# Performance work log

Measured on AMD Instinct MI355X. Metric: run time of the kernel, lower is better.

The kernel has to match this reference:

```python
import jax, jax.numpy as jnp
import numpy as np

B, T, D, H = 4, 2048, 512, 8
K = D // H  # head dim = 64

def setup_inputs() -> dict:
    key = jax.random.key(0)
    k1, k2, k3, k4 = jax.random.split(key, 4)
    x = jax.random.normal(k1, (B, T, D), dtype=jnp.float32)
    # torch nn.Linear stores weight as [out_features, in_features]
    w_qkv = jax.random.normal(k2, (3 * D, D), dtype=jnp.float32) * (D ** -0.5)
    w_proj = jax.random.normal(k3, (D, D), dtype=jnp.float32) * (D ** -0.5)
    b_proj = jax.random.normal(k4, (D,), dtype=jnp.float32) * 0.01
    return {"x": x, "w_qkv": w_qkv, "w_proj": w_proj, "b_proj": b_proj}

def reference(x, w_qkv, w_proj, b_proj):
    Bx, Tx, Dx = x.shape
    # qkv projection (no bias): [B,T,3D]
    qkv = jnp.einsum('btd,ed->bte', x, w_qkv)
    q, k, v = jnp.split(qkv, 3, axis=-1)
    # [B,H,T,K]
    def heads(t):
        return t.reshape(Bx, Tx, H, K).transpose(0, 2, 1, 3)
    q, k, v = heads(q), heads(k), heads(v)
    # scaled scores with causal mask
    scores = jnp.einsum('bhqk,bhsk->bhqs', q, k) * (K ** -0.5)  # [B,H,T,T]
    causal = jnp.tril(jnp.ones((Tx, Tx), dtype=bool))
    scores = jnp.where(causal, scores, -jnp.inf)
    attn = jax.nn.softmax(scores, axis=-1)  # dropout p=0.0 -> identity
    out = jnp.einsum('bhqs,bhsk->bhqk', attn, v)  # [B,H,T,K]
    out = out.transpose(0, 2, 1, 3).reshape(Bx, Tx, Dx)
    out = jnp.einsum('btd,ed->bte', out, w_proj) + b_proj
    return out
```

## Files before the change

### kernel.cpp

```cpp
#include <hip/hip_runtime.h>


typedef unsigned short u16;
typedef __attribute__((ext_vector_type(8))) __bf16 bf16x8;
typedef __attribute__((ext_vector_type(8))) unsigned short u16x8;
typedef __attribute__((ext_vector_type(4))) float f32x4;

#define DEV static __device__ __forceinline__

DEV void async16(const u16* g, u16* l) {
  __builtin_amdgcn_global_load_lds(
      (const __attribute__((address_space(1))) unsigned int*)g,
      (__attribute__((address_space(3))) unsigned int*)l, 16, 0, 0);
}
DEV u16x8 gld8(const u16* p) { return *(const u16x8*)p; }
DEV void lst8(u16* p, u16x8 v) { *(u16x8*)p = v; }
DEV bf16x8 ldsld8(const u16* p) {
  return __builtin_bit_cast(bf16x8, *(const u16x8*)p);
}
DEV f32x4 mfma16(bf16x8 a, bf16x8 b, f32x4 c) {
  return __builtin_amdgcn_mfma_f32_16x16x32_bf16(a, b, c, 0, 0, 0);
}
DEV u16 f2b(float f) {
  unsigned u = __builtin_bit_cast(unsigned, f);
  u += 0x7FFFu + ((u >> 16) & 1u);
  return (u16)(u >> 16);
}
DEV u16x8 pack8(f32x4 a, f32x4 b) {
  u16x8 r;
  r[0] = f2b(a[0]); r[1] = f2b(a[1]); r[2] = f2b(a[2]); r[3] = f2b(a[3]);
  r[4] = f2b(b[0]); r[5] = f2b(b[1]); r[6] = f2b(b[2]); r[7] = f2b(b[3]);
  return r;
}

__global__ void cvt_kernel(const float* __restrict__ in, u16* __restrict__ out,
                           int n8) {
  const int i = blockIdx.x * 256 + threadIdx.x;
  if (i < n8) {
    const float* p = in + (long)i * 8;
    const f32x4 a = *(const f32x4*)p, b = *(const f32x4*)(p + 4);
    *(u16x8*)(out + (long)i * 8) = pack8(a, b);
  }
}

template <typename OutT>
__global__ void gemm_bf16a(const u16* __restrict__ A, const float* __restrict__ Bt,
                           const float* __restrict__ bias, OutT* __restrict__ C,
                           int N, int K) {
  __shared__ __align__(16) u16 As[128 * 32];
  __shared__ __align__(16) u16 Bs[128 * 32];

  const int t = threadIdx.x, lane = t & 63, w = t >> 6;
  const int lane15 = lane & 15, quad = lane >> 4;
  const int wr = w >> 1, wc = w & 1;
  const long row0 = (long)blockIdx.y * 128;
  const int col0 = blockIdx.x * 128;

  const int arow = w * 16 + (lane >> 2), acol = (lane & 3) * 8;
  const u16* Ag = A + (row0 + arow) * (long)K + acol;
  u16* Asw = &As[w * 512];

  const int srow = t >> 2, scol = (t & 3) * 8;
  const float* Bg0 = Bt + (long)(col0 + srow) * K + scol;
  const float* Bg1 = Bg0 + (long)64 * K;
  u16* Bs0 = &Bs[srow * 32 + scol];
  u16* Bs1 = Bs0 + 2048;

  f32x4 acc[4][4];
#pragma unroll
  for (int i = 0; i < 4; i++)
#pragma unroll
    for (int j = 0; j < 4; j++) acc[i][j] = (f32x4)(0.0f);

  f32x4 p0 = *(const f32x4*)Bg0, p1 = *(const f32x4*)(Bg0 + 4);
  f32x4 p2 = *(const f32x4*)Bg1, p3 = *(const f32x4*)(Bg1 + 4);

  for (int k0 = 0; k0 < K; k0 += 32) {
    __syncthreads();
    async16(Ag + k0, Asw);
    async16(Ag + k0 + (long)64 * K, Asw + 2048);
    lst8(Bs0, pack8(p0, p1));
    lst8(Bs1, pack8(p2, p3));
    __syncthreads();

    const int kp = (k0 + 32 < K) ? k0 + 32 : k0;
    p0 = *(const f32x4*)(Bg0 + kp); p1 = *(const f32x4*)(Bg0 + kp + 4);
    p2 = *(const f32x4*)(Bg1 + kp); p3 = *(const f32x4*)(Bg1 + kp + 4);

    bf16x8 a[4], b[4];
#pragma unroll
    for (int i = 0; i < 4; i++)
      a[i] = ldsld8(&As[(wr * 64 + i * 16 + lane15) * 32 + quad * 8]);
#pragma unroll
    for (int j = 0; j < 4; j++)
      b[j] = ldsld8(&Bs[(wc * 64 + j * 16 + lane15) * 32 + quad * 8]);
#pragma unroll
    for (int i = 0; i < 4; i++)
#pragma unroll
      for (int j = 0; j < 4; j++) acc[i][j] = mfma16(a[i], b[j], acc[i][j]);
  }

#pragma unroll
  for (int i = 0; i < 4; i++) {
#pragma unroll
    for (int j = 0; j < 4; j++) {
      const int col = col0 + wc * 64 + j * 16 + lane15;
      const float bv = bias ? bias[col] : 0.0f;
#pragma unroll
      for (int r = 0; r < 4; r++) {
        const long row = row0 + wr * 64 + i * 16 + quad * 4 + r;
        if constexpr (__is_same(OutT, u16))
          C[row * (long)N + col] = f2b(acc[i][j][r] + bv);
        else
          C[row * (long)N + col] = acc[i][j][r] + bv;
      }
    }
  }
}

__global__ void attn_v3(const u16* __restrict__ qkv, u16* __restrict__ out) {
  constexpr int T = 2048, LD = 1536;
  constexpr float CEXP = 0.18033688f;
  __shared__ __align__(16) u16 Ks[64 * 72];
  __shared__ __align__(16) u16 Vt[64 * 72];
  __shared__ __align__(16) u16 Ps[4][16 * 72];

  const int t = threadIdx.x, lane = t & 63, w = t >> 6;
  const int lane15 = lane & 15, quad = lane >> 4;

  const int i = blockIdx.x;
  int qb = i & 31;
  if (i >= 512) qb = 31 - qb;
  const int h = (i >> 5) & 7;
  const int b = (i >> 8) & 3;
  const long base = (long)b * T * LD;

  const u16* gq =
      qkv + base + (long)(qb * 64 + w * 16 + lane15) * LD + h * 64 + quad * 8;
  const bf16x8 qa0 = __builtin_bit_cast(bf16x8, *(const u16x8*)gq);
  const bf16x8 qa1 = __builtin_bit_cast(bf16x8, *(const u16x8*)(gq + 32));

  const int srow = t >> 3, sc8 = (t & 7) * 8;
  const int vs = t >> 2, vd0 = (t & 3) * 16;

  const int nsb = qb + 1;

  u16x8 kr0, kr1, vr0, vr1;
  {
    const u16* gk = qkv + base + (long)srow * LD + 512 + h * 64 + sc8;
    const u16* gv = qkv + base + (long)vs * LD + 1024 + h * 64 + vd0;
    kr0 = gld8(gk); kr1 = gld8(gk + (long)32 * LD);
    vr0 = gld8(gv); vr1 = gld8(gv + 8);
  }

  float lp[4] = {0.0f, 0.0f, 0.0f, 0.0f};
  f32x4 o[4];
#pragma unroll
  for (int j = 0; j < 4; j++) o[j] = (f32x4)(0.0f);

  const int qrow_base = qb * 64 + w * 16 + quad * 4;

  for (int sb = 0; sb < nsb; ++sb) {
    __syncthreads();
    lst8(&Ks[srow * 72 + sc8], kr0);
    lst8(&Ks[(srow + 32) * 72 + sc8], kr1);
#pragma unroll
    for (int ii = 0; ii < 8; ii++) {
      const int d = vd0 + ii;
      Vt[d * 72 + (vs ^ (((d >> 3) & 7) << 3))] = vr0[ii];
    }
#pragma unroll
    for (int ii = 0; ii < 8; ii++) {
      const int d = vd0 + 8 + ii;
      Vt[d * 72 + (vs ^ (((d >> 3) & 7) << 3))] = vr1[ii];
    }
    __syncthreads();

    {
      const int sp = (sb + 1 < nsb) ? sb + 1 : sb;
      const u16* gk = qkv + base + (long)(sp * 64 + srow) * LD + 512 + h * 64 + sc8;
      const u16* gv = qkv + base + (long)(sp * 64 + vs) * LD + 1024 + h * 64 + vd0;
      kr0 = gld8(gk); kr1 = gld8(gk + (long)32 * LD);
      vr0 = gld8(gv); vr1 = gld8(gv + 8);
    }

    f32x4 sf[4];
#pragma unroll
    for (int j = 0; j < 4; j++) {
      f32x4 z = (f32x4)(0.0f);
      z = mfma16(qa0, ldsld8(&Ks[(j * 16 + lane15) * 72 + quad * 8]), z);
      sf[j] = mfma16(qa1, ldsld8(&Ks[(j * 16 + lane15) * 72 + quad * 8 + 32]), z);
    }

    if (sb == qb) {
      const int scol_base = sb * 64 + lane15;
#pragma unroll
      for (int j = 0; j < 4; j++)
#pragma unroll
        for (int r = 0; r < 4; r++) {
          float p = exp2f(sf[j][r] * CEXP);
          if (scol_base + j * 16 > qrow_base + r) p = 0.0f;
          sf[j][r] = p;
          lp[r] += p;
        }
    } else {
#pragma unroll
      for (int j = 0; j < 4; j++)
#pragma unroll
        for (int r = 0; r < 4; r++) {
          const float p = exp2f(sf[j][r] * CEXP);
          sf[j][r] = p;
          lp[r] += p;
        }
    }

    u16* myP = Ps[w];
#pragma unroll
    for (int j = 0; j < 4; j++)
#pragma unroll
      for (int r = 0; r < 4; r++)
        myP[(quad * 4 + r) * 72 + j * 16 + lane15] = f2b(sf[j][r]);
    __asm__ __volatile__("" ::: "memory");
    const bf16x8 pa0 = ldsld8(&myP[lane15 * 72 + quad * 8]);
    const bf16x8 pa1 = ldsld8(&myP[lane15 * 72 + quad * 8 + 32]);
    __asm__ __volatile__("" ::: "memory");

#pragma unroll
    for (int j = 0; j < 4; j++) {
      const int d0 = j * 16 + lane15;
      const int swz = ((d0 >> 3) & 7) << 3;
      o[j] = mfma16(pa0, ldsld8(&Vt[d0 * 72 + ((quad * 8) ^ swz)]), o[j]);
      o[j] = mfma16(pa1, ldsld8(&Vt[d0 * 72 + ((quad * 8 + 32) ^ swz)]), o[j]);
    }
  }

#pragma unroll
  for (int off = 1; off < 16; off <<= 1)
#pragma unroll
    for (int r = 0; r < 4; r++) lp[r] += __shfl_xor(lp[r], off);

  const long orow0 = (long)b * T + qb * 64 + w * 16;
  float inv[4];
#pragma unroll
  for (int r = 0; r < 4; r++) inv[r] = 1.0f / lp[r];
#pragma unroll
  for (int j = 0; j < 4; j++)
#pragma unroll
    for (int r = 0; r < 4; r++)
      out[(orow0 + quad * 4 + r) * 512 + h * 64 + j * 16 + lane15] =
          f2b(o[j][r] * inv[r]);
}

extern "C" void kernel_launch(void* const* d_in, const int* in_sizes, int n_in,
                              void* d_out, int out_size, void* d_ws, size_t ws_size,
                              hipStream_t stream) {
  const float* x      = (const float*)d_in[0];
  const float* w_qkv  = (const float*)d_in[1];
  const float* w_proj = (const float*)d_in[2];
  const float* b_proj = (const float*)d_in[3];
  float* out = (float*)d_out;

  u16* qkv = (u16*)d_ws;
  u16* xb  = qkv + (size_t)8192 * 1536;

  cvt_kernel<<<2048, 256, 0, stream>>>(x, xb, 8192 * 512 / 8);
  gemm_bf16a<u16><<<dim3(12, 64), 256, 0, stream>>>(xb, w_qkv, nullptr, qkv,
                                                    1536, 512);
  attn_v3<<<1024, 256, 0, stream>>>(qkv, xb);
  gemm_bf16a<float><<<dim3(4, 64), 256, 0, stream>>>(xb, w_proj, b_proj, out,
                                                     512, 512);
}
```

Measured before the change: 172.4 us.

## Pre-convert QKV weights to bf16, use K=64 async-loaded GEMM tiles, narrower proj tiles

The conversion kernel now also casts w_qkv to bf16 into scratch space in the output buffer. This lets the QKV GEMM load both operands with async global-to-LDS copies instead of reloading and converting fp32 weights in every block. Both GEMMs now process K in steps of 64 (two 32-wide halves per barrier pair), halving the number of synchronizations. The output projection switches to 128x64 tiles, doubling its grid to 512 blocks for better occupancy. In exchange it adds one extra weight conversion pass and keeps no double buffering across iterations.

```diff
diff --git a/kernel.cpp b/kernel.cpp
--- a/kernel.cpp
+++ b/kernel.cpp
@@ -33,22 +33,25 @@
   return r;
 }
 
-__global__ void cvt_kernel(const float* __restrict__ in, u16* __restrict__ out,
-                           int n8) {
-  const int i = blockIdx.x * 256 + threadIdx.x;
-  if (i < n8) {
-    const float* p = in + (long)i * 8;
-    const f32x4 a = *(const f32x4*)p, b = *(const f32x4*)(p + 4);
-    *(u16x8*)(out + (long)i * 8) = pack8(a, b);
-  }
-}
-
-template <typename OutT>
-__global__ void gemm_bf16a(const u16* __restrict__ A, const float* __restrict__ Bt,
-                           const float* __restrict__ bias, OutT* __restrict__ C,
-                           int N, int K) {
-  __shared__ __align__(16) u16 As[128 * 32];
-  __shared__ __align__(16) u16 Bs[128 * 32];
+__global__ void cvt_all(const float* __restrict__ x, const float* __restrict__ wq,
+                        u16* __restrict__ xb, u16* __restrict__ wqb) {
+  constexpr long NX = 8192L * 512 / 8;
+  constexpr long NQ = 1536L * 512 / 8;
+  const long i = (long)blockIdx.x * 256 + threadIdx.x;
+  if (i < NX) {
+    const float* p = x + i * 8;
+    *(u16x8*)(xb + i * 8) = pack8(*(const f32x4*)p, *(const f32x4*)(p + 4));
+  } else if (i < NX + NQ) {
+    const long j = i - NX;
+    const float* p = wq + j * 8;
+    *(u16x8*)(wqb + j * 8) = pack8(*(const f32x4*)p, *(const f32x4*)(p + 4));
+  }
+}
+
+__global__ void gemm_bb(const u16* __restrict__ A, const u16* __restrict__ Bt,
+                        u16* __restrict__ C, int N, int K) {
+  __shared__ __align__(16) u16 As[2][128 * 32];
+  __shared__ __align__(16) u16 Bs[2][128 * 32];
 
   const int t = threadIdx.x, lane = t & 63, w = t >> 6;
   const int lane15 = lane & 15, quad = lane >> 4;
@@ -56,15 +59,10 @@
   const long row0 = (long)blockIdx.y * 128;
   const int col0 = blockIdx.x * 128;
 
-  const int arow = w * 16 + (lane >> 2), acol = (lane & 3) * 8;
-  const u16* Ag = A + (row0 + arow) * (long)K + acol;
-  u16* Asw = &As[w * 512];
-
-  const int srow = t >> 2, scol = (t & 3) * 8;
-  const float* Bg0 = Bt + (long)(col0 + srow) * K + scol;
-  const float* Bg1 = Bg0 + (long)64 * K;
-  u16* Bs0 = &Bs[srow * 32 + scol];
-  u16* Bs1 = Bs0 + 2048;
+  const int srow = w * 16 + (lane >> 2);
+  const int scol = (lane & 3) * 8;
+  const u16* Ag = A + (row0 + srow) * (long)K + scol;
+  const u16* Bg = Bt + ((long)col0 + srow) * (long)K + scol;
 
   f32x4 acc[4][4];
 #pragma unroll
@@ -72,50 +70,124 @@
 #pragma unroll
     for (int j = 0; j < 4; j++) acc[i][j] = (f32x4)(0.0f);
 
-  f32x4 p0 = *(const f32x4*)Bg0, p1 = *(const f32x4*)(Bg0 + 4);
-  f32x4 p2 = *(const f32x4*)Bg1, p3 = *(const f32x4*)(Bg1 + 4);
-
-  for (int k0 = 0; k0 < K; k0 += 32) {
-    __syncthreads();
-    async16(Ag + k0, Asw);
-    async16(Ag + k0 + (long)64 * K, Asw + 2048);
-    lst8(Bs0, pack8(p0, p1));
-    lst8(Bs1, pack8(p2, p3));
-    __syncthreads();
-
-    const int kp = (k0 + 32 < K) ? k0 + 32 : k0;
-    p0 = *(const f32x4*)(Bg0 + kp); p1 = *(const f32x4*)(Bg0 + kp + 4);
-    p2 = *(const f32x4*)(Bg1 + kp); p3 = *(const f32x4*)(Bg1 + kp + 4);
-
-    bf16x8 a[4], b[4];
-#pragma unroll
-    for (int i = 0; i < 4; i++)
-      a[i] = ldsld8(&As[(wr * 64 + i * 16 + lane15) * 32 + quad * 8]);
-#pragma unroll
-    for (int j = 0; j < 4; j++)
-      b[j] = ldsld8(&Bs[(wc * 64 + j * 16 + lane15) * 32 + quad * 8]);
-#pragma unroll
-    for (int i = 0; i < 4; i++)
-#pragma unroll
-      for (int j = 0; j < 4; j++) acc[i][j] = mfma16(a[i], b[j], acc[i][j]);
-  }
-
-#pragma unroll
-  for (int i = 0; i < 4; i++) {
+  for (int k0 = 0; k0 < K; k0 += 64) {
+    __syncthreads();
+#pragma unroll
+    for (int r = 0; r < 2; r++) {
+#pragma unroll
+      for (int hf = 0; hf < 2; hf++) {
+        async16(Ag + (long)r * 64 * K + k0 + hf * 32,
+                &As[hf][(r * 64 + w * 16) * 32]);
+        async16(Bg + (long)r * 64 * K + k0 + hf * 32,
+                &Bs[hf][(r * 64 + w * 16) * 32]);
+      }
+    }
+    __syncthreads();
+
+#pragma unroll
+    for (int hf = 0; hf < 2; hf++) {
+      bf16x8 a[4], b[4];
+#pragma unroll
+      for (int i = 0; i < 4; i++)
+        a[i] = ldsld8(&As[hf][(wr * 64 + i * 16 + lane15) * 32 + quad * 8]);
+#pragma unroll
+      for (int j = 0; j < 4; j++)
+        b[j] = ldsld8(&Bs[hf][(wc * 64 + j * 16 + lane15) * 32 + quad * 8]);
+#pragma unroll
+      for (int i = 0; i < 4; i++)
+#pragma unroll
+        for (int j = 0; j < 4; j++) acc[i][j] = mfma16(a[i], b[j], acc[i][j]);
+    }
+  }
+
+#pragma unroll
+  for (int i = 0; i < 4; i++)
 #pragma unroll
     for (int j = 0; j < 4; j++) {
       const int col = col0 + wc * 64 + j * 16 + lane15;
-      const float bv = bias ? bias[col] : 0.0f;
 #pragma unroll
       for (int r = 0; r < 4; r++) {
         const long row = row0 + wr * 64 + i * 16 + quad * 4 + r;
-        if constexpr (__is_same(OutT, u16))
-          C[row * (long)N + col] = f2b(acc[i][j][r] + bv);
-        else
-          C[row * (long)N + col] = acc[i][j][r] + bv;
+        C[row * (long)N + col] = f2b(acc[i][j][r]);
       }
     }
-  }
+}
+
+__global__ void gemm_b64(const u16* __restrict__ A, const float* __restrict__ Bt,
+                         const float* __restrict__ bias, float* __restrict__ C,
+                         int N, int K) {
+  __shared__ __align__(16) u16 As[2][128 * 32];
+  __shared__ __align__(16) u16 Bs[2][64 * 32];
+
+  const int t = threadIdx.x, lane = t & 63, w = t >> 6;
+  const int lane15 = lane & 15, quad = lane >> 4;
+  const int wr = w >> 1, wc = w & 1;
+  const long row0 = (long)blockIdx.y * 128;
+  const int col0 = blockIdx.x * 64;
+
+  const int srow = w * 16 + (lane >> 2);
+  const int scol = (lane & 3) * 8;
+  const u16* Ag = A + (row0 + srow) * (long)K + scol;
+
+  const int brow = t >> 2, bc = (t & 3) * 16;
+  const float* Bg = Bt + (long)(col0 + brow) * K + bc;
+  u16* BsD = &Bs[bc >> 5][brow * 32 + (bc & 31)];
+
+  f32x4 acc[4][2];
+#pragma unroll
+  for (int i = 0; i < 4; i++)
+#pragma unroll
+    for (int j = 0; j < 2; j++) acc[i][j] = (f32x4)(0.0f);
+
+  f32x4 q0 = *(const f32x4*)Bg, q1 = *(const f32x4*)(Bg + 4);
+  f32x4 q2 = *(const f32x4*)(Bg + 8), q3 = *(const f32x4*)(Bg + 12);
+
+  for (int k0 = 0; k0 < K; k0 += 64) {
+    __syncthreads();
+#pragma unroll
+    for (int r = 0; r < 2; r++)
+#pragma unroll
+      for (int hf = 0; hf < 2; hf++)
+        async16(Ag + (long)r * 64 * K + k0 + hf * 32,
+                &As[hf][(r * 64 + w * 16) * 32]);
+    lst8(BsD, pack8(q0, q1));
+    lst8(BsD + 8, pack8(q2, q3));
+    __syncthreads();
+
+    {
+      const int kp = (k0 + 64 < K) ? k0 + 64 : k0;
+      q0 = *(const f32x4*)(Bg + kp);     q1 = *(const f32x4*)(Bg + kp + 4);
+      q2 = *(const f32x4*)(Bg + kp + 8); q3 = *(const f32x4*)(Bg + kp + 12);
+    }
+
+#pragma unroll
+    for (int hf = 0; hf < 2; hf++) {
+      bf16x8 a[4], b[2];
+#pragma unroll
+      for (int i = 0; i < 4; i++)
+        a[i] = ldsld8(&As[hf][(wr * 64 + i * 16 + lane15) * 32 + quad * 8]);
+#pragma unroll
+      for (int j = 0; j < 2; j++)
+        b[j] = ldsld8(&Bs[hf][(wc * 32 + j * 16 + lane15) * 32 + quad * 8]);
+#pragma unroll
+      for (int i = 0; i < 4; i++)
+#pragma unroll
+        for (int j = 0; j < 2; j++) acc[i][j] = mfma16(a[i], b[j], acc[i][j]);
+    }
+  }
+
+#pragma unroll
+  for (int i = 0; i < 4; i++)
+#pragma unroll
+    for (int j = 0; j < 2; j++) {
+      const int col = col0 + wc * 32 + j * 16 + lane15;
+      const float bv = bias[col];
+#pragma unroll
+      for (int r = 0; r < 4; r++) {
+        const long row = row0 + wr * 64 + i * 16 + quad * 4 + r;
+        C[row * (long)N + col] = acc[i][j][r] + bv;
+      }
+    }
 }
 
 __global__ void attn_v3(const u16* __restrict__ qkv, u16* __restrict__ out) {
@@ -262,11 +334,10 @@
 
   u16* qkv = (u16*)d_ws;
   u16* xb  = qkv + (size_t)8192 * 1536;
-
-  cvt_kernel<<<2048, 256, 0, stream>>>(x, xb, 8192 * 512 / 8);
-  gemm_bf16a<u16><<<dim3(12, 64), 256, 0, stream>>>(xb, w_qkv, nullptr, qkv,
-                                                    1536, 512);
+  u16* wqb = (u16*)d_out;
+
+  cvt_all<<<2432, 256, 0, stream>>>(x, w_qkv, xb, wqb);
+  gemm_bb<<<dim3(12, 64), 256, 0, stream>>>(xb, wqb, qkv, 1536, 512);
   attn_v3<<<1024, 256, 0, stream>>>(qkv, xb);
-  gemm_bf16a<float><<<dim3(4, 64), 256, 0, stream>>>(xb, w_proj, b_proj, out,
-                                                     512, 512);
-}
+  gemm_b64<<<dim3(8, 64), 256, 0, stream>>>(xb, w_proj, b_proj, out, 512, 512);
+}
```

New measurement: 163.8 us. 5.0% less time.
